# Kernel tuning notes

Hardware: AMD Instinct MI355X
Metric: run time of the kernel (lower is better)

## Reference

```python
import jax, jax.numpy as jnp
import numpy as np

B, C, H, W = 4, 256, 64, 64
CQ = C // 8


def setup_inputs() -> dict:
    key = jax.random.key(0)
    ks = jax.random.split(key, 7)
    x = jax.random.normal(ks[0], (B, C, H, W), dtype=jnp.float32)
    Wq = jax.random.normal(ks[1], (CQ, C), dtype=jnp.float32) * 0.02
    bq = jnp.zeros((CQ,), dtype=jnp.float32)
    Wk = jax.random.normal(ks[2], (CQ, C), dtype=jnp.float32) * 0.02
    bk = jnp.zeros((CQ,), dtype=jnp.float32)
    Wv = jax.random.normal(ks[3], (C, C), dtype=jnp.float32) * 0.02
    bv = jnp.zeros((C,), dtype=jnp.float32)
    return {"x": x, "Wq": Wq, "bq": bq, "Wk": Wk, "bk": bk, "Wv": Wv, "bv": bv}


def reference(x, Wq, bq, Wk, bk, Wv, bv):
    b, c, h, w = x.shape
    n = h * w
    xf = x.reshape(b, c, n)                                   # [B,C,N]
    # 1x1 convs are per-pixel GEMMs
    q = jnp.einsum('qc,bcn->bnq', Wq, xf) + bq                # [B,N,Cq]
    k = jnp.einsum('qc,bcn->bqn', Wk, xf) + bk[None, :, None] # [B,Cq,N]
    v = jnp.einsum('vc,bcn->bnv', Wv, xf) + bv                # [B,N,C]
    scale = float(n) ** 0.5
    energy = jnp.einsum('bnq,bqm->bnm', q, k) / scale         # [B,N,N]
    attn = jax.nn.softmax(energy, axis=-1)
    out = jnp.einsum('bnm,bmv->bnv', attn, v)                 # [B,N,C]
    # Faithful to torch's out.view(B,C,H,W) applied to the contiguous [B,N,C]
    # tensor: a raw memory reinterpretation, NOT a transpose.
    return out.reshape(b, c, h, w)
```

## Files before the change

### kernel.cpp

```cpp
#include <hip/hip_runtime.h>

#define BATCH 4
#define CH    256
#define NPIX  4096
#define CQD   32

typedef __bf16 bf16;
typedef bf16 bf16x8 __attribute__((ext_vector_type(8)));
typedef bf16 bf16x4 __attribute__((ext_vector_type(4)));
typedef float f32x4 __attribute__((ext_vector_type(4)));

#define MFMA16 __builtin_amdgcn_mfma_f32_16x16x32_bf16

#define GLOAD_LDS16(g, l) __builtin_amdgcn_global_load_lds( \
    (const __attribute__((address_space(1))) void*)(g),     \
    (__attribute__((address_space(3))) void*)(l), 16, 0, 0)

__global__ __launch_bounds__(256) void prep_kernel(
    const float* __restrict__ Wq, const float* __restrict__ bq,
    const float* __restrict__ Wk, const float* __restrict__ bk,
    const float* __restrict__ Wv, const float* __restrict__ bv,
    bf16* __restrict__ Wb, float* __restrict__ bb)
{
    int r = blockIdx.x, c = threadIdx.x;
    const float* W; const float* bs; float sc; int rr;
    if (r < 32)      { W = Wq; bs = bq; sc = 0.015625f; rr = r; }
    else if (r < 64) { W = Wk; bs = bk; sc = 1.0f;      rr = r - 32; }
    else             { W = Wv; bs = bv; sc = 1.0f;      rr = r - 64; }
    Wb[(size_t)r * CH + c] = (bf16)(W[(size_t)rr * CH + c] * sc);
    if (c == 0) bb[r] = bs[rr] * sc;
}

__global__ __launch_bounds__(256) void proj_kernel(
    const float* __restrict__ x,
    const bf16* __restrict__ Wb, const float* __restrict__ bb,
    bf16* __restrict__ qp, bf16* __restrict__ kp, bf16* __restrict__ vT)
{
    __shared__ __align__(16) bf16 xT[32][264];
    __shared__ __align__(16) bf16 vstage[4][16][40];

    const int t  = threadIdx.x;
    const int b  = blockIdx.x >> 7;
    const int n0 = (blockIdx.x & 127) << 5;
    const int w    = t >> 6;
    const int lane = t & 63;
    const int l16  = t & 15;
    const int quad = (t & 63) >> 4;

    const float* xb = x + (size_t)b * CH * NPIX;
#pragma unroll
    for (int j = 0; j < 8; ++j) {
        int id = t + j * 256;
        int c  = id >> 3;
        int n4 = (id & 7) << 2;
        float4 vv = *(const float4*)(xb + (size_t)c * NPIX + n0 + n4);
        xT[n4 + 0][c] = (bf16)vv.x;
        xT[n4 + 1][c] = (bf16)vv.y;
        xT[n4 + 2][c] = (bf16)vv.z;
        xT[n4 + 3][c] = (bf16)vv.w;
    }
    __syncthreads();

    for (int rt = 0; rt < 5; ++rt) {
        int ro = w * 80 + rt * 16;
        int kind = (ro < 32) ? 0 : (ro < 64) ? 1 : 2;

        bf16x8 afrag[8];
        const bf16* wrow = Wb + (size_t)(ro + l16) * CH + quad * 8;
#pragma unroll
        for (int kc = 0; kc < 8; ++kc)
            afrag[kc] = *(const bf16x8*)(wrow + kc * 32);
        float bv4[4];
#pragma unroll
        for (int r = 0; r < 4; ++r) bv4[r] = bb[ro + quad * 4 + r];

#pragma unroll
        for (int nt = 0; nt < 2; ++nt) {
            f32x4 acc = {0.f, 0.f, 0.f, 0.f};
#pragma unroll
            for (int kc = 0; kc < 8; ++kc) {
                bf16x8 bfr = *(const bf16x8*)&xT[nt * 16 + l16][kc * 32 + quad * 8];
                acc = MFMA16(afrag[kc], bfr, acc, 0, 0, 0);
            }
            if (kind != 2) {
                bf16x4 pk;
#pragma unroll
                for (int r = 0; r < 4; ++r)
                    pk[r] = (bf16)(acc[r] + bv4[r]);
                int n = n0 + nt * 16 + l16;
                int col = (kind == 0 ? ro : ro - 32) + quad * 4;
                bf16* dst = (kind == 0) ? qp : kp;
                *(bf16x4*)&dst[((size_t)b * NPIX + n) * CQD + col] = pk;
            } else {
#pragma unroll
                for (int r = 0; r < 4; ++r)
                    vstage[w][quad * 4 + r][nt * 16 + l16] = (bf16)(acc[r] + bv4[r]);
            }
        }
        if (kind == 2) {
            int vrow = lane >> 2, vcc = lane & 3;
            bf16x8 chunk = *(const bf16x8*)&vstage[w][vrow][vcc * 8];
            *(bf16x8*)&vT[((size_t)b * CH + (ro - 64) + vrow) * NPIX + n0 + vcc * 8] = chunk;
        }
    }
}

template<int S, bool DIRECT>
__global__ __launch_bounds__(256, 2) void attn_kernel(
    const bf16* __restrict__ qp, const bf16* __restrict__ kp,
    const bf16* __restrict__ vT,
    bf16* __restrict__ Opart, float* __restrict__ Lpart,
    float* __restrict__ out)
{
    __shared__ __align__(16) bf16 Vt[2][256][64];
    __shared__ __align__(16) bf16 Pb[4][2][16][64];

    const int t    = threadIdx.x;
    const int bid  = blockIdx.x;
    const int s    = bid % S;
    const int tq   = bid / S;
    const int b    = tq >> 5;
    const int qt   = tq & 31;
    const int n0   = qt << 7;
    const int w    = t >> 6;
    const int lane = t & 63;
    const int l16  = t & 15;
    const int quad = (t & 63) >> 4;
    const int sw   = l16 & 7;

    const bf16* qpb = qp + ((size_t)b * NPIX + n0 + w * 32) * CQD;
    bf16x8 qfrag[2];
    qfrag[0] = *(const bf16x8*)(qpb + (size_t)l16 * CQD + quad * 8);
    qfrag[1] = *(const bf16x8*)(qpb + (size_t)(16 + l16) * CQD + quad * 8);

    f32x4 o[2][16];
#pragma unroll
    for (int g = 0; g < 2; ++g)
#pragma unroll
        for (int ct = 0; ct < 16; ++ct) o[g][ct] = (f32x4){0.f, 0.f, 0.f, 0.f};
    float lsum[2] = {0.f, 0.f};

    const bf16* kpb = kp + (size_t)b * NPIX * CQD;
    const bf16* vTb = vT + (size_t)b * CH * NPIX;
    const int k0 = s * (NPIX / S);
    const int iters = NPIX / S / 64;

    const int vrow_off = lane >> 3;
    const int vchunk   = (lane & 7) ^ vrow_off;
    auto issue_vt = [&](int buf, int m0) {
#pragma unroll
        for (int j = 0; j < 8; ++j) {
            int rowbase = j * 32 + w * 8;
            const bf16* src = vTb + (size_t)(rowbase + vrow_off) * NPIX + m0 + vchunk * 8;
            GLOAD_LDS16(src, &Vt[buf][rowbase][0]);
        }
    };
    auto load_kf = [&](int m0, bf16x8* kf) {
#pragma unroll
        for (int mt = 0; mt < 4; ++mt)
            kf[mt] = *(const bf16x8*)(kpb + (size_t)(m0 + mt * 16 + l16) * CQD + quad * 8);
    };

    bf16x8 kfa[4], kfb[4];
    issue_vt(0, k0);
    load_kf(k0, kfa);
    __syncthreads();

    for (int mi = 0; mi < iters; ++mi) {
        const int cur = mi & 1;
        if (mi + 1 < iters) {
            issue_vt(cur ^ 1, k0 + ((mi + 1) << 6));
            load_kf(k0 + ((mi + 1) << 6), kfb);
        }

        f32x4 sv[2][4];
#pragma unroll
        for (int mt = 0; mt < 4; ++mt) {
            f32x4 z = {0.f, 0.f, 0.f, 0.f};
            sv[0][mt] = MFMA16(kfa[mt], qfrag[0], z, 0, 0, 0);
            sv[1][mt] = MFMA16(kfa[mt], qfrag[1], z, 0, 0, 0);
        }

#pragma unroll
        for (int g = 0; g < 2; ++g) {
            float rs = 0.f;
#pragma unroll
            for (int mt = 0; mt < 4; ++mt) {
                bf16x4 pk;
#pragma unroll
                for (int r = 0; r < 4; ++r) {
                    float e = __expf(sv[g][mt][r]);
                    rs += e;
                    pk[r] = (bf16)e;
                }
                int slot = (2 * mt + (quad >> 1)) ^ sw;
                *(bf16x4*)&Pb[w][g][l16][slot * 8 + (quad & 1) * 4] = pk;
            }
            lsum[g] += rs;
        }
        bf16x8 pf[2][2];
#pragma unroll
        for (int g = 0; g < 2; ++g)
#pragma unroll
            for (int kc = 0; kc < 2; ++kc) {
                int slot = (4 * kc + quad) ^ sw;
                pf[g][kc] = *(const bf16x8*)&Pb[w][g][l16][slot * 8];
            }

#pragma unroll
        for (int ct = 0; ct < 16; ++ct) {
            int row = ct * 16 + l16;
            bf16x8 v0 = *(const bf16x8*)&Vt[cur][row][((quad) ^ sw) * 8];
            bf16x8 v1 = *(const bf16x8*)&Vt[cur][row][((4 + quad) ^ sw) * 8];
            o[0][ct] = MFMA16(pf[0][0], v0, o[0][ct], 0, 0, 0);
            o[0][ct] = MFMA16(pf[0][1], v1, o[0][ct], 0, 0, 0);
            o[1][ct] = MFMA16(pf[1][0], v0, o[1][ct], 0, 0, 0);
            o[1][ct] = MFMA16(pf[1][1], v1, o[1][ct], 0, 0, 0);
        }
        __syncthreads();
#pragma unroll
        for (int i = 0; i < 4; ++i) kfa[i] = kfb[i];
    }

    float l_g[2];
#pragma unroll
    for (int g = 0; g < 2; ++g) {
        float v = lsum[g];
        v += __shfl_xor(v, 16);
        v += __shfl_xor(v, 32);
        l_g[g] = v;
    }

    if (!DIRECT) {
        const size_t prb = (((size_t)s * BATCH + b) * 32 + qt) * 128 + w * 32;
        if (quad == 0) {
#pragma unroll
            for (int g = 0; g < 2; ++g)
                Lpart[prb + g * 16 + l16] = l_g[g];
        }
        bf16* eb = &Pb[w][0][0][0];
#pragma unroll
        for (int g = 0; g < 2; ++g) {
            float rinv[4];
#pragma unroll
            for (int r = 0; r < 4; ++r) rinv[r] = 1.0f / __shfl(l_g[g], quad * 4 + r);
#pragma unroll
            for (int h = 0; h < 4; ++h) {
#pragma unroll
                for (int c2 = 0; c2 < 4; ++c2) {
                    int ct = h * 4 + c2;
#pragma unroll
                    for (int r = 0; r < 4; ++r)
                        eb[(quad * 4 + r) * 72 + c2 * 16 + l16] =
                            (bf16)(o[g][ct][r] * rinv[r]);
                }
                int vrow = lane >> 3, vcc = lane & 7;
#pragma unroll
                for (int pass = 0; pass < 2; ++pass) {
                    bf16x8 chunk = *(const bf16x8*)&eb[(pass * 8 + vrow) * 72 + vcc * 8];
                    *(bf16x8*)&Opart[(prb + g * 16 + pass * 8 + vrow) * CH +
                                     h * 64 + vcc * 8] = chunk;
                }
            }
        }
    } else {
        float* ob = out + ((size_t)b * NPIX + n0 + w * 32) * CH;
#pragma unroll
        for (int g = 0; g < 2; ++g) {
            float rinv[4];
#pragma unroll
            for (int r = 0; r < 4; ++r) rinv[r] = 1.0f / __shfl(l_g[g], quad * 4 + r);
#pragma unroll
            for (int ct = 0; ct < 16; ++ct)
#pragma unroll
                for (int r = 0; r < 4; ++r)
                    ob[(size_t)(g * 16 + quad * 4 + r) * CH + ct * 16 + l16] =
                        o[g][ct][r] * rinv[r];
        }
    }
}

template<int S>
__global__ __launch_bounds__(256) void combine_kernel(
    const bf16* __restrict__ Opart, const float* __restrict__ Lpart,
    float* __restrict__ out)
{
    int idx  = blockIdx.x * 256 + threadIdx.x;
    int nrow = idx >> 5;
    int cc   = (idx & 31) * 8;
    int b    = nrow >> 12, nin = nrow & 4095;
    int qt   = nin >> 7,  rl  = nin & 127;

    size_t pr[S];
    float  ls[S], wsum = 0.f;
#pragma unroll
    for (int s = 0; s < S; ++s) {
        pr[s] = (((size_t)s * BATCH + b) * 32 + qt) * 128 + rl;
        ls[s] = Lpart[pr[s]];
        wsum += ls[s];
    }
    float inv = 1.0f / wsum;

    float acc[8] = {0.f, 0.f, 0.f, 0.f, 0.f, 0.f, 0.f, 0.f};
#pragma unroll
    for (int s = 0; s < S; ++s) {
        bf16x8 ov = *(const bf16x8*)&Opart[pr[s] * CH + cc];
        float wn = ls[s] * inv;
#pragma unroll
        for (int j = 0; j < 8; ++j) acc[j] += wn * (float)ov[j];
    }
    float4 o0 = {acc[0], acc[1], acc[2], acc[3]};
    float4 o1 = {acc[4], acc[5], acc[6], acc[7]};
    *(float4*)&out[(size_t)nrow * CH + cc]     = o0;
    *(float4*)&out[(size_t)nrow * CH + cc + 4] = o1;
}

extern "C" void kernel_launch(void* const* d_in, const int* in_sizes, int n_in,
                              void* d_out, int out_size, void* d_ws, size_t ws_size,
                              hipStream_t stream) {
    const float* x  = (const float*)d_in[0];
    const float* Wq = (const float*)d_in[1];
    const float* bq = (const float*)d_in[2];
    const float* Wk = (const float*)d_in[3];
    const float* bk = (const float*)d_in[4];
    const float* Wv = (const float*)d_in[5];
    const float* bv = (const float*)d_in[6];
    float* out = (float*)d_out;

    char* ws = (char*)d_ws;
    const size_t qpB   = (size_t)BATCH * NPIX * CQD * 2;
    const size_t vTB   = (size_t)BATCH * CH * NPIX * 2;
    const size_t WbB   = (size_t)320 * CH * 2;
    const size_t bbB   = 320 * 4 + 768;
    const size_t baseB = 2 * qpB + vTB + WbB + bbB;
    const size_t oprtB = (size_t)BATCH * NPIX * CH * 2;
    const size_t mlB   = (size_t)BATCH * NPIX * 4;

    bf16*  qp = (bf16*)ws;
    bf16*  kp = (bf16*)(ws + qpB);
    bf16*  vT = (bf16*)(ws + 2 * qpB);
    bf16*  Wb = (bf16*)(ws + 2 * qpB + vTB);
    float* bb = (float*)(ws + 2 * qpB + vTB + WbB);

    prep_kernel<<<dim3(320), dim3(256), 0, stream>>>(Wq, bq, Wk, bk, Wv, bv, Wb, bb);
    proj_kernel<<<dim3(BATCH * (NPIX / 32)), dim3(256), 0, stream>>>(
        x, Wb, bb, qp, kp, vT);

    auto need = [&](int S) { return baseB + (size_t)S * (oprtB + mlB); };
    int S = (ws_size >= need(4)) ? 4 : (ws_size >= need(2)) ? 2
          : (ws_size >= need(1)) ? 1 : 0;

    if (S > 0) {
        bf16*  Opart = (bf16*)(ws + baseB);
        float* Lpart = (float*)(ws + baseB + (size_t)S * oprtB);
        if (S == 4) {
            attn_kernel<4, false><<<dim3(128 * 4), dim3(256), 0, stream>>>(
                qp, kp, vT, Opart, Lpart, out);
            combine_kernel<4><<<dim3(2048), dim3(256), 0, stream>>>(Opart, Lpart, out);
        } else if (S == 2) {
            attn_kernel<2, false><<<dim3(128 * 2), dim3(256), 0, stream>>>(
                qp, kp, vT, Opart, Lpart, out);
            combine_kernel<2><<<dim3(2048), dim3(256), 0, stream>>>(Opart, Lpart, out);
        } else {
            attn_kernel<1, false><<<dim3(128), dim3(256), 0, stream>>>(
                qp, kp, vT, Opart, Lpart, out);
            combine_kernel<1><<<dim3(2048), dim3(256), 0, stream>>>(Opart, Lpart, out);
        }
    } else {
        attn_kernel<1, true><<<dim3(128), dim3(256), 0, stream>>>(
            qp, kp, vT, nullptr, nullptr, out);
    }
}
```

Measured before the change: 142.0 us.

## Halve attention query and key tiles, split value channels across wave pairs

Restructures the attention kernel to use 64-query blocks instead of 128. Four waves now form two query groups by two channel halves, and the key step shrinks from 64 to 32. This halves shared memory and accumulator registers so three blocks fit per CU, and it doubles the grid to fill the MI355X's many CUs. The cost is that each K/V tile is reused by fewer queries, so V traffic per block roughly doubles, and synchronisation per unit of work goes up. The partial-output layout and the combine kernel's indexing are updated to match.

```diff
diff --git a/kernel.cpp b/kernel.cpp
--- a/kernel.cpp
+++ b/kernel.cpp
@@ -106,62 +106,64 @@
 }
 
 template<int S, bool DIRECT>
-__global__ __launch_bounds__(256, 2) void attn_kernel(
+__global__ __launch_bounds__(256, 3) void attn_kernel(
     const bf16* __restrict__ qp, const bf16* __restrict__ kp,
     const bf16* __restrict__ vT,
     bf16* __restrict__ Opart, float* __restrict__ Lpart,
     float* __restrict__ out)
 {
-    __shared__ __align__(16) bf16 Vt[2][256][64];
-    __shared__ __align__(16) bf16 Pb[4][2][16][64];
+    __shared__ __align__(16) bf16 Vt[2][256][32];
+    __shared__ __align__(16) bf16 Pb[4][2][16][32];
 
     const int t    = threadIdx.x;
     const int bid  = blockIdx.x;
     const int s    = bid % S;
     const int tq   = bid / S;
-    const int b    = tq >> 5;
-    const int qt   = tq & 31;
-    const int n0   = qt << 7;
+    const int b    = tq >> 6;
+    const int qt   = tq & 63;
+    const int n0   = qt << 6;
     const int w    = t >> 6;
+    const int qg   = w >> 1;
+    const int cg   = w & 1;
     const int lane = t & 63;
     const int l16  = t & 15;
     const int quad = (t & 63) >> 4;
-    const int sw   = l16 & 7;
-
-    const bf16* qpb = qp + ((size_t)b * NPIX + n0 + w * 32) * CQD;
+    const int sw   = l16 & 3;
+
+    const bf16* qpb = qp + ((size_t)b * NPIX + n0 + qg * 32) * CQD;
     bf16x8 qfrag[2];
     qfrag[0] = *(const bf16x8*)(qpb + (size_t)l16 * CQD + quad * 8);
     qfrag[1] = *(const bf16x8*)(qpb + (size_t)(16 + l16) * CQD + quad * 8);
 
-    f32x4 o[2][16];
+    f32x4 o[2][8];
 #pragma unroll
     for (int g = 0; g < 2; ++g)
 #pragma unroll
-        for (int ct = 0; ct < 16; ++ct) o[g][ct] = (f32x4){0.f, 0.f, 0.f, 0.f};
+        for (int ct = 0; ct < 8; ++ct) o[g][ct] = (f32x4){0.f, 0.f, 0.f, 0.f};
     float lsum[2] = {0.f, 0.f};
 
     const bf16* kpb = kp + (size_t)b * NPIX * CQD;
     const bf16* vTb = vT + (size_t)b * CH * NPIX;
     const int k0 = s * (NPIX / S);
-    const int iters = NPIX / S / 64;
-
-    const int vrow_off = lane >> 3;
-    const int vchunk   = (lane & 7) ^ vrow_off;
+    const int iters = NPIX / S / 32;
+
+    const int vrow_off = lane >> 2;
+    const int vchunk   = (lane & 3) ^ (vrow_off & 3);
     auto issue_vt = [&](int buf, int m0) {
 #pragma unroll
-        for (int j = 0; j < 8; ++j) {
-            int rowbase = j * 32 + w * 8;
+        for (int j = 0; j < 4; ++j) {
+            int rowbase = w * 64 + j * 16;
             const bf16* src = vTb + (size_t)(rowbase + vrow_off) * NPIX + m0 + vchunk * 8;
             GLOAD_LDS16(src, &Vt[buf][rowbase][0]);
         }
     };
     auto load_kf = [&](int m0, bf16x8* kf) {
 #pragma unroll
-        for (int mt = 0; mt < 4; ++mt)
+        for (int mt = 0; mt < 2; ++mt)
             kf[mt] = *(const bf16x8*)(kpb + (size_t)(m0 + mt * 16 + l16) * CQD + quad * 8);
     };
 
-    bf16x8 kfa[4], kfb[4];
+    bf16x8 kfa[2], kfb[2];
     issue_vt(0, k0);
     load_kf(k0, kfa);
     __syncthreads();
@@ -169,23 +171,24 @@
     for (int mi = 0; mi < iters; ++mi) {
         const int cur = mi & 1;
         if (mi + 1 < iters) {
-            issue_vt(cur ^ 1, k0 + ((mi + 1) << 6));
-            load_kf(k0 + ((mi + 1) << 6), kfb);
-        }
-
-        f32x4 sv[2][4];
-#pragma unroll
-        for (int mt = 0; mt < 4; ++mt) {
+            issue_vt(cur ^ 1, k0 + ((mi + 1) << 5));
+            load_kf(k0 + ((mi + 1) << 5), kfb);
+        }
+
+        f32x4 sv[2][2];
+#pragma unroll
+        for (int mt = 0; mt < 2; ++mt) {
             f32x4 z = {0.f, 0.f, 0.f, 0.f};
             sv[0][mt] = MFMA16(kfa[mt], qfrag[0], z, 0, 0, 0);
             sv[1][mt] = MFMA16(kfa[mt], qfrag[1], z, 0, 0, 0);
         }
 
+        bf16x8 pf[2];
 #pragma unroll
         for (int g = 0; g < 2; ++g) {
             float rs = 0.f;
 #pragma unroll
-            for (int mt = 0; mt < 4; ++mt) {
+            for (int mt = 0; mt < 2; ++mt) {
                 bf16x4 pk;
 #pragma unroll
                 for (int r = 0; r < 4; ++r) {
@@ -198,28 +201,20 @@
             }
             lsum[g] += rs;
         }
-        bf16x8 pf[2][2];
 #pragma unroll
         for (int g = 0; g < 2; ++g)
-#pragma unroll
-            for (int kc = 0; kc < 2; ++kc) {
-                int slot = (4 * kc + quad) ^ sw;
-                pf[g][kc] = *(const bf16x8*)&Pb[w][g][l16][slot * 8];
-            }
-
-#pragma unroll
-        for (int ct = 0; ct < 16; ++ct) {
-            int row = ct * 16 + l16;
-            bf16x8 v0 = *(const bf16x8*)&Vt[cur][row][((quad) ^ sw) * 8];
-            bf16x8 v1 = *(const bf16x8*)&Vt[cur][row][((4 + quad) ^ sw) * 8];
-            o[0][ct] = MFMA16(pf[0][0], v0, o[0][ct], 0, 0, 0);
-            o[0][ct] = MFMA16(pf[0][1], v1, o[0][ct], 0, 0, 0);
-            o[1][ct] = MFMA16(pf[1][0], v0, o[1][ct], 0, 0, 0);
-            o[1][ct] = MFMA16(pf[1][1], v1, o[1][ct], 0, 0, 0);
+            pf[g] = *(const bf16x8*)&Pb[w][g][l16][(quad ^ sw) * 8];
+
+#pragma unroll
+        for (int ct = 0; ct < 8; ++ct) {
+            int row = cg * 128 + ct * 16 + l16;
+            bf16x8 v = *(const bf16x8*)&Vt[cur][row][(quad ^ sw) * 8];
+            o[0][ct] = MFMA16(pf[0], v, o[0][ct], 0, 0, 0);
+            o[1][ct] = MFMA16(pf[1], v, o[1][ct], 0, 0, 0);
         }
         __syncthreads();
 #pragma unroll
-        for (int i = 0; i < 4; ++i) kfa[i] = kfb[i];
+        for (int i = 0; i < 2; ++i) kfa[i] = kfb[i];
     }
 
     float l_g[2];
@@ -232,46 +227,41 @@
     }
 
     if (!DIRECT) {
-        const size_t prb = (((size_t)s * BATCH + b) * 32 + qt) * 128 + w * 32;
-        if (quad == 0) {
+        const size_t prb = ((size_t)s * BATCH + b) * NPIX + n0 + qg * 32;
+        if (cg == 0 && quad == 0) {
 #pragma unroll
             for (int g = 0; g < 2; ++g)
                 Lpart[prb + g * 16 + l16] = l_g[g];
         }
-        bf16* eb = &Pb[w][0][0][0];
+        bf16* eb = (bf16*)Vt + (size_t)w * 16 * 136;
 #pragma unroll
         for (int g = 0; g < 2; ++g) {
             float rinv[4];
 #pragma unroll
             for (int r = 0; r < 4; ++r) rinv[r] = 1.0f / __shfl(l_g[g], quad * 4 + r);
 #pragma unroll
-            for (int h = 0; h < 4; ++h) {
-#pragma unroll
-                for (int c2 = 0; c2 < 4; ++c2) {
-                    int ct = h * 4 + c2;
-#pragma unroll
-                    for (int r = 0; r < 4; ++r)
-                        eb[(quad * 4 + r) * 72 + c2 * 16 + l16] =
-                            (bf16)(o[g][ct][r] * rinv[r]);
-                }
-                int vrow = lane >> 3, vcc = lane & 7;
-#pragma unroll
-                for (int pass = 0; pass < 2; ++pass) {
-                    bf16x8 chunk = *(const bf16x8*)&eb[(pass * 8 + vrow) * 72 + vcc * 8];
-                    *(bf16x8*)&Opart[(prb + g * 16 + pass * 8 + vrow) * CH +
-                                     h * 64 + vcc * 8] = chunk;
-                }
+            for (int ct = 0; ct < 8; ++ct)
+#pragma unroll
+                for (int r = 0; r < 4; ++r)
+                    eb[(quad * 4 + r) * 136 + ct * 16 + l16] =
+                        (bf16)(o[g][ct][r] * rinv[r]);
+            int vrow = lane >> 4, vcc = lane & 15;
+#pragma unroll
+            for (int pass = 0; pass < 4; ++pass) {
+                bf16x8 chunk = *(const bf16x8*)&eb[(pass * 4 + vrow) * 136 + vcc * 8];
+                *(bf16x8*)&Opart[(prb + g * 16 + pass * 4 + vrow) * CH +
+                                 cg * 128 + vcc * 8] = chunk;
             }
         }
     } else {
-        float* ob = out + ((size_t)b * NPIX + n0 + w * 32) * CH;
+        float* ob = out + ((size_t)b * NPIX + n0 + qg * 32) * CH + cg * 128;
 #pragma unroll
         for (int g = 0; g < 2; ++g) {
             float rinv[4];
 #pragma unroll
             for (int r = 0; r < 4; ++r) rinv[r] = 1.0f / __shfl(l_g[g], quad * 4 + r);
 #pragma unroll
-            for (int ct = 0; ct < 16; ++ct)
+            for (int ct = 0; ct < 8; ++ct)
 #pragma unroll
                 for (int r = 0; r < 4; ++r)
                     ob[(size_t)(g * 16 + quad * 4 + r) * CH + ct * 16 + l16] =
@@ -289,13 +279,12 @@
     int nrow = idx >> 5;
     int cc   = (idx & 31) * 8;
     int b    = nrow >> 12, nin = nrow & 4095;
-    int qt   = nin >> 7,  rl  = nin & 127;
 
     size_t pr[S];
     float  ls[S], wsum = 0.f;
 #pragma unroll
     for (int s = 0; s < S; ++s) {
-        pr[s] = (((size_t)s * BATCH + b) * 32 + qt) * 128 + rl;
+        pr[s] = ((size_t)s * BATCH + b) * NPIX + nin;
         ls[s] = Lpart[pr[s]];
         wsum += ls[s];
     }
@@ -354,20 +343,20 @@
         bf16*  Opart = (bf16*)(ws + baseB);
         float* Lpart = (float*)(ws + baseB + (size_t)S * oprtB);
         if (S == 4) {
-            attn_kernel<4, false><<<dim3(128 * 4), dim3(256), 0, stream>>>(
+            attn_kernel<4, false><<<dim3(256 * 4), dim3(256), 0, stream>>>(
                 qp, kp, vT, Opart, Lpart, out);
             combine_kernel<4><<<dim3(2048), dim3(256), 0, stream>>>(Opart, Lpart, out);
         } else if (S == 2) {
-            attn_kernel<2, false><<<dim3(128 * 2), dim3(256), 0, stream>>>(
+            attn_kernel<2, false><<<dim3(256 * 2), dim3(256), 0, stream>>>(
                 qp, kp, vT, Opart, Lpart, out);
             combine_kernel<2><<<dim3(2048), dim3(256), 0, stream>>>(Opart, Lpart, out);
         } else {
-            attn_kernel<1, false><<<dim3(128), dim3(256), 0, stream>>>(
+            attn_kernel<1, false><<<dim3(256), dim3(256), 0, stream>>>(
                 qp, kp, vT, Opart, Lpart, out);
             combine_kernel<1><<<dim3(2048), dim3(256), 0, stream>>>(Opart, Lpart, out);
         }
     } else {
-        attn_kernel<1, true><<<dim3(128), dim3(256), 0, stream>>>(
+        attn_kernel<1, true><<<dim3(256), dim3(256), 0, stream>>>(
             qp, kp, vT, nullptr, nullptr, out);
     }
 }
```

Result: slower. 178.7 us (+25.8%).

## Switch PV product to 32x32x16 MFMA with block-shared P tile

Applied to the files above, without the earlier changes.

Each wave previously computed all 256 output channels for its own 32 query rows using 16x16x32 MFMAs. Now the exp'd score tile is written to one shared LDS buffer for the whole block, and each wave computes a 64-query by 128-channel output tile using 32x32x16 MFMAs. Fewer, larger MFMAs mean fewer V-tile LDS reads per FLOP. The cost is an extra block-wide barrier each iteration and a reworked epilogue, which stages row sums through LDS and writes Opart in a new plain row-major layout.

```diff
diff --git a/kernel.cpp b/kernel.cpp
--- a/kernel.cpp
+++ b/kernel.cpp
@@ -9,8 +9,10 @@
 typedef bf16 bf16x8 __attribute__((ext_vector_type(8)));
 typedef bf16 bf16x4 __attribute__((ext_vector_type(4)));
 typedef float f32x4 __attribute__((ext_vector_type(4)));
+typedef float f32x16 __attribute__((ext_vector_type(16)));
 
 #define MFMA16 __builtin_amdgcn_mfma_f32_16x16x32_bf16
+#define MFMA32 __builtin_amdgcn_mfma_f32_32x32x16_bf16
 
 #define GLOAD_LDS16(g, l) __builtin_amdgcn_global_load_lds( \
     (const __attribute__((address_space(1))) void*)(g),     \
@@ -113,7 +115,7 @@
     float* __restrict__ out)
 {
     __shared__ __align__(16) bf16 Vt[2][256][64];
-    __shared__ __align__(16) bf16 Pb[4][2][16][64];
+    __shared__ __align__(16) bf16 PbS[128][64];
 
     const int t    = threadIdx.x;
     const int bid  = blockIdx.x;
@@ -127,17 +129,23 @@
     const int l16  = t & 15;
     const int quad = (t & 63) >> 4;
     const int sw   = l16 & 7;
+    const int l32  = lane & 31;
+    const int h    = lane >> 5;
+    const int qh   = w >> 1;
+    const int chb  = (w & 1) * 128;
 
     const bf16* qpb = qp + ((size_t)b * NPIX + n0 + w * 32) * CQD;
     bf16x8 qfrag[2];
     qfrag[0] = *(const bf16x8*)(qpb + (size_t)l16 * CQD + quad * 8);
     qfrag[1] = *(const bf16x8*)(qpb + (size_t)(16 + l16) * CQD + quad * 8);
 
-    f32x4 o[2][16];
-#pragma unroll
-    for (int g = 0; g < 2; ++g)
-#pragma unroll
-        for (int ct = 0; ct < 16; ++ct) o[g][ct] = (f32x4){0.f, 0.f, 0.f, 0.f};
+    f32x16 o[2][4];
+#pragma unroll
+    for (int i = 0; i < 2; ++i)
+#pragma unroll
+        for (int j = 0; j < 4; ++j)
+#pragma unroll
+            for (int r = 0; r < 16; ++r) o[i][j][r] = 0.f;
     float lsum[2] = {0.f, 0.f};
 
     const bf16* kpb = kp + (size_t)b * NPIX * CQD;
@@ -168,9 +176,10 @@
 
     for (int mi = 0; mi < iters; ++mi) {
         const int cur = mi & 1;
+        const int m0  = k0 + (mi << 6);
         if (mi + 1 < iters) {
-            issue_vt(cur ^ 1, k0 + ((mi + 1) << 6));
-            load_kf(k0 + ((mi + 1) << 6), kfb);
+            issue_vt(cur ^ 1, m0 + 64);
+            load_kf(m0 + 64, kfb);
         }
 
         f32x4 sv[2][4];
@@ -194,28 +203,32 @@
                     pk[r] = (bf16)e;
                 }
                 int slot = (2 * mt + (quad >> 1)) ^ sw;
-                *(bf16x4*)&Pb[w][g][l16][slot * 8 + (quad & 1) * 4] = pk;
+                *(bf16x4*)&PbS[w * 32 + g * 16 + l16][slot * 8 + (quad & 1) * 4] = pk;
             }
             lsum[g] += rs;
         }
-        bf16x8 pf[2][2];
-#pragma unroll
-        for (int g = 0; g < 2; ++g)
-#pragma unroll
-            for (int kc = 0; kc < 2; ++kc) {
-                int slot = (4 * kc + quad) ^ sw;
-                pf[g][kc] = *(const bf16x8*)&Pb[w][g][l16][slot * 8];
-            }
-
-#pragma unroll
-        for (int ct = 0; ct < 16; ++ct) {
-            int row = ct * 16 + l16;
-            bf16x8 v0 = *(const bf16x8*)&Vt[cur][row][((quad) ^ sw) * 8];
-            bf16x8 v1 = *(const bf16x8*)&Vt[cur][row][((4 + quad) ^ sw) * 8];
-            o[0][ct] = MFMA16(pf[0][0], v0, o[0][ct], 0, 0, 0);
-            o[0][ct] = MFMA16(pf[0][1], v1, o[0][ct], 0, 0, 0);
-            o[1][ct] = MFMA16(pf[1][0], v0, o[1][ct], 0, 0, 0);
-            o[1][ct] = MFMA16(pf[1][1], v1, o[1][ct], 0, 0, 0);
+        __syncthreads();
+
+        bf16x8 pA[2][4];
+#pragma unroll
+        for (int t32 = 0; t32 < 2; ++t32)
+#pragma unroll
+            for (int kg = 0; kg < 4; ++kg) {
+                int row = qh * 64 + t32 * 32 + l32;
+                pA[t32][kg] = *(const bf16x8*)&PbS[row][((2 * kg + h) ^ (l32 & 7)) * 8];
+            }
+#pragma unroll
+        for (int ct = 0; ct < 4; ++ct) {
+            int vrow = chb + ct * 32 + l32;
+            bf16x8 vB[4];
+#pragma unroll
+            for (int kg = 0; kg < 4; ++kg)
+                vB[kg] = *(const bf16x8*)&Vt[cur][vrow][((2 * kg + h) ^ (l32 & 7)) * 8];
+#pragma unroll
+            for (int t32 = 0; t32 < 2; ++t32)
+#pragma unroll
+                for (int kg = 0; kg < 4; ++kg)
+                    o[t32][ct] = MFMA32(pA[t32][kg], vB[kg], o[t32][ct], 0, 0, 0);
         }
         __syncthreads();
 #pragma unroll
@@ -230,52 +243,55 @@
         v += __shfl_xor(v, 32);
         l_g[g] = v;
     }
-
-    if (!DIRECT) {
-        const size_t prb = (((size_t)s * BATCH + b) * 32 + qt) * 128 + w * 32;
-        if (quad == 0) {
-#pragma unroll
-            for (int g = 0; g < 2; ++g)
-                Lpart[prb + g * 16 + l16] = l_g[g];
-        }
-        bf16* eb = &Pb[w][0][0][0];
-#pragma unroll
-        for (int g = 0; g < 2; ++g) {
-            float rinv[4];
-#pragma unroll
-            for (int r = 0; r < 4; ++r) rinv[r] = 1.0f / __shfl(l_g[g], quad * 4 + r);
-#pragma unroll
-            for (int h = 0; h < 4; ++h) {
-#pragma unroll
-                for (int c2 = 0; c2 < 4; ++c2) {
-                    int ct = h * 4 + c2;
-#pragma unroll
-                    for (int r = 0; r < 4; ++r)
-                        eb[(quad * 4 + r) * 72 + c2 * 16 + l16] =
-                            (bf16)(o[g][ct][r] * rinv[r]);
+    float* lsh = (float*)PbS;
+    if (quad == 0) {
+#pragma unroll
+        for (int g = 0; g < 2; ++g)
+            lsh[w * 32 + g * 16 + l16] = l_g[g];
+    }
+    __syncthreads();
+
+    const size_t prb2 = ((size_t)s * BATCH + b) * NPIX + n0;
+    if (!DIRECT && quad == 0) {
+#pragma unroll
+        for (int g = 0; g < 2; ++g)
+            Lpart[prb2 + w * 32 + g * 16 + l16] = l_g[g];
+    }
+
+    bf16* eb = (bf16*)Vt + (size_t)w * 32 * 136;
+#pragma unroll
+    for (int t32 = 0; t32 < 2; ++t32) {
+        float rinv[16];
+#pragma unroll
+        for (int reg = 0; reg < 16; ++reg) {
+            int q_r = (reg & 3) + 8 * (reg >> 2) + 4 * h;
+            rinv[reg] = 1.0f / lsh[qh * 64 + t32 * 32 + q_r];
+        }
+        if (!DIRECT) {
+#pragma unroll
+            for (int ct = 0; ct < 4; ++ct)
+#pragma unroll
+                for (int reg = 0; reg < 16; ++reg) {
+                    int q_r = (reg & 3) + 8 * (reg >> 2) + 4 * h;
+                    eb[q_r * 136 + ct * 32 + l32] = (bf16)(o[t32][ct][reg] * rinv[reg]);
                 }
-                int vrow = lane >> 3, vcc = lane & 7;
-#pragma unroll
-                for (int pass = 0; pass < 2; ++pass) {
-                    bf16x8 chunk = *(const bf16x8*)&eb[(pass * 8 + vrow) * 72 + vcc * 8];
-                    *(bf16x8*)&Opart[(prb + g * 16 + pass * 8 + vrow) * CH +
-                                     h * 64 + vcc * 8] = chunk;
+            int vrow = lane >> 4, vcc = lane & 15;
+#pragma unroll
+            for (int p = 0; p < 8; ++p) {
+                int row = p * 4 + vrow;
+                bf16x8 chunk = *(const bf16x8*)&eb[row * 136 + vcc * 8];
+                *(bf16x8*)&Opart[(prb2 + qh * 64 + t32 * 32 + row) * CH +
+                                 chb + vcc * 8] = chunk;
+            }
+        } else {
+            float* ob = out + (prb2 + qh * 64 + t32 * 32) * CH + chb;
+#pragma unroll
+            for (int ct = 0; ct < 4; ++ct)
+#pragma unroll
+                for (int reg = 0; reg < 16; ++reg) {
+                    int q_r = (reg & 3) + 8 * (reg >> 2) + 4 * h;
+                    ob[(size_t)q_r * CH + ct * 32 + l32] = o[t32][ct][reg] * rinv[reg];
                 }
-            }
-        }
-    } else {
-        float* ob = out + ((size_t)b * NPIX + n0 + w * 32) * CH;
-#pragma unroll
-        for (int g = 0; g < 2; ++g) {
-            float rinv[4];
-#pragma unroll
-            for (int r = 0; r < 4; ++r) rinv[r] = 1.0f / __shfl(l_g[g], quad * 4 + r);
-#pragma unroll
-            for (int ct = 0; ct < 16; ++ct)
-#pragma unroll
-                for (int r = 0; r < 4; ++r)
-                    ob[(size_t)(g * 16 + quad * 4 + r) * CH + ct * 16 + l16] =
-                        o[g][ct][r] * rinv[r];
         }
     }
 }
@@ -289,13 +305,12 @@
     int nrow = idx >> 5;
     int cc   = (idx & 31) * 8;
     int b    = nrow >> 12, nin = nrow & 4095;
-    int qt   = nin >> 7,  rl  = nin & 127;
 
     size_t pr[S];
     float  ls[S], wsum = 0.f;
 #pragma unroll
     for (int s = 0; s < S; ++s) {
-        pr[s] = (((size_t)s * BATCH + b) * 32 + qt) * 128 + rl;
+        pr[s] = ((size_t)s * BATCH + b) * NPIX + nin;
         ls[s] = Lpart[pr[s]];
         wsum += ls[s];
     }
```

Result: no change. 140.9 us (-0.8%).
